# Kernel tuning notes

Measured on AMD Instinct MI355X. Metric: run time of the kernel, lower is better.

## Reference

```python
import jax, jax.numpy as jnp
import numpy as np

B, C, D, H, W = 4, 256, 16, 64, 64


def setup_inputs() -> dict:
    key = jax.random.key(0)
    ks = jax.random.split(key, 9)
    s = 1.0 / np.sqrt(C)
    return {
        "x": jax.random.normal(ks[0], (B, C, H, W), dtype=jnp.float32),
        "Wq": jax.random.normal(ks[1], (D, C), dtype=jnp.float32) * s,
        "bq": jax.random.normal(ks[2], (D,), dtype=jnp.float32) * 0.01,
        "Wk": jax.random.normal(ks[3], (D, C), dtype=jnp.float32) * s,
        "bk": jax.random.normal(ks[4], (D,), dtype=jnp.float32) * 0.01,
        "Wv": jax.random.normal(ks[5], (D, C), dtype=jnp.float32) * s,
        "bv": jax.random.normal(ks[6], (D,), dtype=jnp.float32) * 0.01,
        "Wo": jax.random.normal(ks[7], (C, D), dtype=jnp.float32) / np.sqrt(D),
        "bo": jax.random.normal(ks[8], (C,), dtype=jnp.float32) * 0.01,
    }


def reference(x, Wq, bq, Wk, bk, Wv, bv, Wo, bo):
    b, c, h, w = x.shape
    n = h * w
    xf = x.reshape(b, c, n)                                   # [B,C,N]
    # 1x1 convs == channel-mixing matmuls
    q = jnp.einsum("bcn,dc->bdn", xf, Wq) + bq[:, None]        # [B,D,N]
    k = jnp.einsum("bcn,dc->bdn", xf, Wk) + bk[:, None]
    v = jnp.einsum("bcn,dc->bdn", xf, Wv) + bv[:, None]
    # attention_map[b, i, j] = softmax_j(q_i . k_j)  (NO 1/sqrt(d) scale)
    scores = jnp.einsum("bdi,bdj->bij", q, k)                  # [B,N,N]
    attn = jax.nn.softmax(scores, axis=-1)
    # attended[b, d, i] = sum_j v[b,d,j] * attn[b,i,j]
    av = jnp.einsum("bdj,bij->bdi", v, attn)                   # [B,D,N]
    out = jnp.einsum("bdn,cd->bcn", av, Wo) + bo[:, None]      # [B,C,N]
    return out.reshape(b, c, h, w)
```

## Files before the change

### kernel.cpp

```cpp
#include <hip/hip_runtime.h>
#include <hip/hip_bf16.h>

typedef unsigned short u16;
typedef unsigned int u32;
typedef float f32x4 __attribute__((ext_vector_type(4)));
typedef short bf16x8 __attribute__((ext_vector_type(8)));

#define LOG2E 1.4426950408889634f

static __device__ __forceinline__ u16 f2bf(float f){
  __hip_bfloat16 h = __float2bfloat16(f);
  return __builtin_bit_cast(u16, h);
}
static __device__ __forceinline__ float bf2f(u16 u){
  __hip_bfloat16 h = __builtin_bit_cast(__hip_bfloat16, u);
  return __bfloat162float(h);
}
static __device__ __forceinline__ float fexp2(float x){
#if __has_builtin(__builtin_amdgcn_exp2f)
  return __builtin_amdgcn_exp2f(x);
#else
  return exp2f(x);
#endif
}
static __device__ __forceinline__ u32 pack2(float a, float b){
  return (u32)f2bf(a) | ((u32)f2bf(b) << 16);
}
static __device__ __forceinline__ f32x4 mf(bf16x8 a, bf16x8 b, f32x4 c){
  return __builtin_amdgcn_mfma_f32_16x16x32_bf16(a, b, c, 0, 0, 0);
}

__global__ __launch_bounds__(256, 2) void qkv_kernel(
    const float* __restrict__ x,
    const float* __restrict__ Wq, const float* __restrict__ bq,
    const float* __restrict__ Wk, const float* __restrict__ bk,
    const float* __restrict__ Wv, const float* __restrict__ bv,
    u16* __restrict__ qh, u16* __restrict__ ql,
    u16* __restrict__ kcat, u16* __restrict__ khz, u16* __restrict__ vT)
{
  __shared__ float wlds[48*256];
  int t = threadIdx.x;
  int nt = blockIdx.x, b = blockIdx.y;
  for (int idx = t; idx < 48*256; idx += 256) {
    int o = idx >> 8, c = idx & 255;
    int m = o >> 4, d = o & 15;
    const float* W = (m==0) ? Wq : (m==1) ? Wk : Wv;
    int cg = c >> 6, cc4 = (c >> 2) & 15, j = c & 3;
    int pos = (o << 8) + (cg << 6) + (((cc4 ^ cg) & 15) << 2) + j;
    wlds[pos] = W[d*256 + c];
  }
  __syncthreads();
  int w = t >> 6, lane = t & 63;
  int nl = lane & 15, cg = lane >> 4;
  int n = nt*64 + w*16 + nl;
  float acc[48];
  #pragma unroll
  for (int o = 0; o < 48; ++o) acc[o] = 0.f;
  const float* xb = x + (b << 20) + n;
  const float4* wl4 = (const float4*)wlds;
  #pragma unroll 2
  for (int cc4 = 0; cc4 < 16; ++cc4) {
    int c0 = cg*64 + cc4*4;
    float x0 = xb[(c0+0) << 12];
    float x1 = xb[(c0+1) << 12];
    float x2 = xb[(c0+2) << 12];
    float x3 = xb[(c0+3) << 12];
    int f4b = (cg << 4) + (cc4 ^ cg);
    #pragma unroll
    for (int o = 0; o < 48; ++o) {
      float4 wv = wl4[(o << 6) + f4b];
      acc[o] += wv.x*x0 + wv.y*x1 + wv.z*x2 + wv.w*x3;
    }
  }
  #pragma unroll
  for (int o = 0; o < 48; ++o) {
    acc[o] += __shfl_xor(acc[o], 16, 64);
    acc[o] += __shfl_xor(acc[o], 32, 64);
  }
  if (cg == 0) {
    alignas(16) u16 hq[16]; alignas(16) u16 lq[16];
    #pragma unroll
    for (int d = 0; d < 16; ++d) {
      float v_ = acc[d] + bq[d];
      u16 h = f2bf(v_);
      hq[d] = h;
      lq[d] = f2bf(v_ - bf2f(h));
    }
    int4* dst = (int4*)(qh + ((size_t)((b << 12) + n))*16);
    dst[0] = ((int4*)hq)[0]; dst[1] = ((int4*)hq)[1];
    int4* dst2 = (int4*)(ql + ((size_t)((b << 12) + n))*16);
    dst2[0] = ((int4*)lq)[0]; dst2[1] = ((int4*)lq)[1];
  } else if (cg == 1) {
    alignas(16) u16 kk[32]; alignas(16) u16 kz2[32];
    #pragma unroll
    for (int d = 0; d < 16; ++d) {
      float v_ = acc[16+d] + bk[d];
      u16 h = f2bf(v_);
      u16 l_ = f2bf(v_ - bf2f(h));
      kk[d] = h; kk[16+d] = l_;
      kz2[d] = h; kz2[16+d] = 0;
    }
    int4* dst = (int4*)(kcat + ((size_t)((b << 12) + n))*32);
    #pragma unroll
    for (int q_ = 0; q_ < 4; ++q_) dst[q_] = ((int4*)kk)[q_];
    int4* dst2 = (int4*)(khz + ((size_t)((b << 12) + n))*32);
    #pragma unroll
    for (int q_ = 0; q_ < 4; ++q_) dst2[q_] = ((int4*)kz2)[q_];
  } else if (cg == 2) {
    #pragma unroll
    for (int d = 0; d < 16; ++d) {
      float v_ = acc[32+d] + bv[d];
      vT[((size_t)((b*16 + d) << 12)) + n] = f2bf(v_);
    }
  }
}

struct Frags { bf16x8 ac0,ac1,ac2,ac3, az0,az1,az2,az3, v0,v1; };

static __device__ __forceinline__ Frags loadFrags(
  const u16* __restrict__ kc, const u16* __restrict__ kz,
  const u16* __restrict__ vp, int kb, int i, int g)
{
  Frags f;
  const u16* a0 = kc + (kb + i)*32 + g*8;
  f.ac0 = *(const bf16x8*)(a0);
  f.ac1 = *(const bf16x8*)(a0 + 512);
  f.ac2 = *(const bf16x8*)(a0 + 1024);
  f.ac3 = *(const bf16x8*)(a0 + 1536);
  const u16* z0 = kz + (kb + i)*32 + g*8;
  f.az0 = *(const bf16x8*)(z0);
  f.az1 = *(const bf16x8*)(z0 + 512);
  f.az2 = *(const bf16x8*)(z0 + 1024);
  f.az3 = *(const bf16x8*)(z0 + 1536);
  const u16* v0p = vp + kb + g*8;
  f.v0 = *(const bf16x8*)(v0p);
  f.v1 = *(const bf16x8*)(v0p + 32);
  return f;
}

__global__ __launch_bounds__(256, 2) void attn_kernel(
    const u16* __restrict__ qh, const u16* __restrict__ ql,
    const u16* __restrict__ kcat, const u16* __restrict__ khz,
    const u16* __restrict__ vT,
    float* __restrict__ av_part, float* __restrict__ l_part)
{
  __shared__ char plds[4*2048];
  int tid = threadIdx.x, wid = tid >> 6, lane = tid & 63;
  int g = lane >> 4, i = lane & 15;
  int b = blockIdx.y, s = blockIdx.z;
  int qidx = blockIdx.x*64 + wid*16 + i;
  char* myp = plds + wid*2048;
  int rowb = i*128;
  int mi = (i & 7) << 4;

  bf16x8 Bqh = *(const bf16x8*)(qh + ((size_t)((b << 12) + qidx))*16 + ((g & 1) << 3));
  bf16x8 Bql = *(const bf16x8*)(ql + ((size_t)((b << 12) + qidx))*16 + ((g & 1) << 3));
  const u16* kc = kcat + (size_t)b*4096*32;
  const u16* kz = khz  + (size_t)b*4096*32;
  const u16* vp = vT   + ((size_t)(b*16 + i) << 12);

  f32x4 av = {0.f,0.f,0.f,0.f};
  float lsum = 0.f;
  int kb0 = s*2048;
  Frags cu = loadFrags(kc, kz, vp, kb0, i, g);
  #pragma unroll 2
  for (int it = 0; it < 32; ++it) {
    int kb = kb0 + it*64;
    int kbn = (it < 31) ? (kb + 64) : kb;
    Frags nx = loadFrags(kc, kz, vp, kbn, i, g);
    f32x4 z4 = {0.f,0.f,0.f,0.f};
    f32x4 s0 = mf(cu.ac0, Bqh, z4); s0 = mf(cu.az0, Bql, s0);
    f32x4 s1 = mf(cu.ac1, Bqh, z4); s1 = mf(cu.az1, Bql, s1);
    f32x4 s2 = mf(cu.ac2, Bqh, z4); s2 = mf(cu.az2, Bql, s2);
    f32x4 s3 = mf(cu.ac3, Bqh, z4); s3 = mf(cu.az3, Bql, s3);
    f32x4 p0, p1, p2, p3;
    #pragma unroll
    for (int r = 0; r < 4; ++r) {
      p0[r] = fexp2(s0[r]*LOG2E);
      p1[r] = fexp2(s1[r]*LOG2E);
      p2[r] = fexp2(s2[r]*LOG2E);
      p3[r] = fexp2(s3[r]*LOG2E);
    }
    lsum += (p0[0]+p0[1]+p0[2]+p0[3]) + (p1[0]+p1[1]+p1[2]+p1[3])
          + (p2[0]+p2[1]+p2[2]+p2[3]) + (p3[0]+p3[1]+p3[2]+p3[3]);
    *(uint2*)(myp + rowb + (((8*g)      ) ^ mi)) =
        (uint2){ pack2(p0[0], p0[1]), pack2(p0[2], p0[3]) };
    *(uint2*)(myp + rowb + (((8*g) + 32 ) ^ mi)) =
        (uint2){ pack2(p1[0], p1[1]), pack2(p1[2], p1[3]) };
    *(uint2*)(myp + rowb + (((8*g) + 64 ) ^ mi)) =
        (uint2){ pack2(p2[0], p2[1]), pack2(p2[2], p2[3]) };
    *(uint2*)(myp + rowb + (((8*g) + 96 ) ^ mi)) =
        (uint2){ pack2(p3[0], p3[1]), pack2(p3[2], p3[3]) };
    bf16x8 Bp0 = *(const bf16x8*)(myp + rowb + (( 0 + 16*g) ^ mi));
    bf16x8 Bp1 = *(const bf16x8*)(myp + rowb + ((64 + 16*g) ^ mi));
    av = mf(cu.v0, Bp0, av);
    av = mf(cu.v1, Bp1, av);
    cu = nx;
  }
  float lt = lsum;
  lt += __shfl_xor(lt, 16, 64);
  lt += __shfl_xor(lt, 32, 64);
  float* avp = av_part + ((size_t)((s*4 + b)*16) << 12);
  #pragma unroll
  for (int r = 0; r < 4; ++r)
    avp[((size_t)(4*g + r) << 12) + qidx] = av[r];
  if (lane < 16)
    l_part[((size_t)((s*4 + b)) << 12) + qidx] = lt;
}

__global__ __launch_bounds__(256, 4) void outproj_kernel(
    const float* __restrict__ av_part, const float* __restrict__ l_part,
    const float* __restrict__ Wo, const float* __restrict__ bo,
    float* __restrict__ out)
{
  __shared__ float wl[16][16];
  __shared__ float bol[16];
  int t = threadIdx.x;
  int ct = blockIdx.x, ntile = blockIdx.y, b = blockIdx.z;
  wl[t >> 4][t & 15] = Wo[(ct*16 + (t >> 4))*16 + (t & 15)];
  if (t < 16) bol[t] = bo[ct*16 + t];
  __syncthreads();
  int n = ntile*256 + t;
  float l0 = l_part[((size_t)b << 12) + n];
  float l1 = l_part[((size_t)(4 + b) << 12) + n];
  float inv = 1.f / (l0 + l1);
  float avv[16];
  #pragma unroll
  for (int d = 0; d < 16; ++d) {
    float a0 = av_part[((size_t)(b*16 + d) << 12) + n];
    float a1 = av_part[((size_t)((4 + b)*16 + d) << 12) + n];
    avv[d] = (a0 + a1) * inv;
  }
  #pragma unroll
  for (int cc = 0; cc < 16; ++cc) {
    float o = bol[cc];
    #pragma unroll
    for (int d = 0; d < 16; ++d) o += wl[cc][d] * avv[d];
    out[((size_t)(b*256 + ct*16 + cc) << 12) + n] = o;
  }
}

extern "C" void kernel_launch(void* const* d_in, const int* in_sizes, int n_in,
                              void* d_out, int out_size, void* d_ws, size_t ws_size,
                              hipStream_t stream) {
  (void)in_sizes; (void)n_in; (void)out_size; (void)ws_size;
  const float* x  = (const float*)d_in[0];
  const float* Wq = (const float*)d_in[1];
  const float* bq = (const float*)d_in[2];
  const float* Wk = (const float*)d_in[3];
  const float* bk = (const float*)d_in[4];
  const float* Wv = (const float*)d_in[5];
  const float* bv = (const float*)d_in[6];
  const float* Wo = (const float*)d_in[7];
  const float* bo = (const float*)d_in[8];
  float* out = (float*)d_out;
  char* ws = (char*)d_ws;

  u16* qh   = (u16*)(ws + 0);
  u16* ql   = (u16*)(ws + 524288);
  u16* kcat = (u16*)(ws + 1048576);
  u16* khz  = (u16*)(ws + 2097152);
  u16* vT   = (u16*)(ws + 3145728);
  float* av_part = (float*)(ws + 3670016);
  float* l_part  = (float*)(ws + 5767168);

  qkv_kernel<<<dim3(64, 4), dim3(256), 0, stream>>>(
      x, Wq, bq, Wk, bk, Wv, bv, qh, ql, kcat, khz, vT);
  attn_kernel<<<dim3(64, 4, 2), dim3(256), 0, stream>>>(
      qh, ql, kcat, khz, vT, av_part, l_part);
  outproj_kernel<<<dim3(16, 16, 4), dim3(256), 0, stream>>>(
      av_part, l_part, Wo, bo, out);
}
```

Baseline: 159.5 us.

## Split QKV projection across grid, drop khz buffer, raise attention key-split count

The QKV kernel now launches one grid slice per projection (q, k, v), each holding only 16 output weights in LDS and 16 accumulators. This cuts register and LDS pressure and triples the block count. The separate zero-padded K buffer is removed: the attention kernel reuses the kcat fragments and zeroes the low-Q operand for the upper lane groups, which halves K fragment loads. The key dimension is split up to 8 ways, chosen from workspace size, and outproj reduces over a variable number of partial results, adding more partial-sum traffic in exchange for more parallel blocks.

```diff
diff --git a/kernel.cpp b/kernel.cpp
--- a/kernel.cpp
+++ b/kernel.cpp
@@ -36,29 +36,29 @@
     const float* __restrict__ Wk, const float* __restrict__ bk,
     const float* __restrict__ Wv, const float* __restrict__ bv,
     u16* __restrict__ qh, u16* __restrict__ ql,
-    u16* __restrict__ kcat, u16* __restrict__ khz, u16* __restrict__ vT)
-{
-  __shared__ float wlds[48*256];
+    u16* __restrict__ kcat, u16* __restrict__ vT)
+{
+  __shared__ float wlds[16*256];
   int t = threadIdx.x;
-  int nt = blockIdx.x, b = blockIdx.y;
-  for (int idx = t; idx < 48*256; idx += 256) {
-    int o = idx >> 8, c = idx & 255;
-    int m = o >> 4, d = o & 15;
-    const float* W = (m==0) ? Wq : (m==1) ? Wk : Wv;
+  int nt = blockIdx.x, b = blockIdx.y, m = blockIdx.z;
+  const float* W    = (m==0) ? Wq : (m==1) ? Wk : Wv;
+  const float* bias = (m==0) ? bq : (m==1) ? bk : bv;
+  for (int idx = t; idx < 16*256; idx += 256) {
+    int d = idx >> 8, c = idx & 255;
     int cg = c >> 6, cc4 = (c >> 2) & 15, j = c & 3;
-    int pos = (o << 8) + (cg << 6) + (((cc4 ^ cg) & 15) << 2) + j;
+    int pos = (d << 8) + (cg << 6) + ((cc4 ^ cg) << 2) + j;
     wlds[pos] = W[d*256 + c];
   }
   __syncthreads();
   int w = t >> 6, lane = t & 63;
   int nl = lane & 15, cg = lane >> 4;
   int n = nt*64 + w*16 + nl;
-  float acc[48];
-  #pragma unroll
-  for (int o = 0; o < 48; ++o) acc[o] = 0.f;
+  float acc[16];
+  #pragma unroll
+  for (int d = 0; d < 16; ++d) acc[d] = 0.f;
   const float* xb = x + (b << 20) + n;
   const float4* wl4 = (const float4*)wlds;
-  #pragma unroll 2
+  #pragma unroll 4
   for (int cc4 = 0; cc4 < 16; ++cc4) {
     int c0 = cg*64 + cc4*4;
     float x0 = xb[(c0+0) << 12];
@@ -67,59 +67,48 @@
     float x3 = xb[(c0+3) << 12];
     int f4b = (cg << 4) + (cc4 ^ cg);
     #pragma unroll
-    for (int o = 0; o < 48; ++o) {
-      float4 wv = wl4[(o << 6) + f4b];
-      acc[o] += wv.x*x0 + wv.y*x1 + wv.z*x2 + wv.w*x3;
-    }
-  }
-  #pragma unroll
-  for (int o = 0; o < 48; ++o) {
-    acc[o] += __shfl_xor(acc[o], 16, 64);
-    acc[o] += __shfl_xor(acc[o], 32, 64);
-  }
-  if (cg == 0) {
-    alignas(16) u16 hq[16]; alignas(16) u16 lq[16];
-    #pragma unroll
     for (int d = 0; d < 16; ++d) {
-      float v_ = acc[d] + bq[d];
+      float4 wv = wl4[(d << 6) + f4b];
+      acc[d] += wv.x*x0 + wv.y*x1 + wv.z*x2 + wv.w*x3;
+    }
+  }
+  #pragma unroll
+  for (int d = 0; d < 16; ++d) {
+    acc[d] += __shfl_xor(acc[d], 16, 64);
+    acc[d] += __shfl_xor(acc[d], 32, 64);
+  }
+  if (m == 2) {
+    #pragma unroll
+    for (int jj = 0; jj < 4; ++jj) {
+      int d = cg*4 + jj;
+      vT[((size_t)((b*16 + d)) << 12) + n] = f2bf(acc[d] + bias[d]);
+    }
+  } else {
+    int d0 = (cg & 1) * 8, lo = cg >> 1;
+    alignas(16) u16 vals[8];
+    #pragma unroll
+    for (int jj = 0; jj < 8; ++jj) {
+      int d = d0 + jj;
+      float v_ = acc[d] + bias[d];
       u16 h = f2bf(v_);
-      hq[d] = h;
-      lq[d] = f2bf(v_ - bf2f(h));
-    }
-    int4* dst = (int4*)(qh + ((size_t)((b << 12) + n))*16);
-    dst[0] = ((int4*)hq)[0]; dst[1] = ((int4*)hq)[1];
-    int4* dst2 = (int4*)(ql + ((size_t)((b << 12) + n))*16);
-    dst2[0] = ((int4*)lq)[0]; dst2[1] = ((int4*)lq)[1];
-  } else if (cg == 1) {
-    alignas(16) u16 kk[32]; alignas(16) u16 kz2[32];
-    #pragma unroll
-    for (int d = 0; d < 16; ++d) {
-      float v_ = acc[16+d] + bk[d];
-      u16 h = f2bf(v_);
-      u16 l_ = f2bf(v_ - bf2f(h));
-      kk[d] = h; kk[16+d] = l_;
-      kz2[d] = h; kz2[16+d] = 0;
-    }
-    int4* dst = (int4*)(kcat + ((size_t)((b << 12) + n))*32);
-    #pragma unroll
-    for (int q_ = 0; q_ < 4; ++q_) dst[q_] = ((int4*)kk)[q_];
-    int4* dst2 = (int4*)(khz + ((size_t)((b << 12) + n))*32);
-    #pragma unroll
-    for (int q_ = 0; q_ < 4; ++q_) dst2[q_] = ((int4*)kz2)[q_];
-  } else if (cg == 2) {
-    #pragma unroll
-    for (int d = 0; d < 16; ++d) {
-      float v_ = acc[32+d] + bv[d];
-      vT[((size_t)((b*16 + d) << 12)) + n] = f2bf(v_);
-    }
-  }
-}
-
-struct Frags { bf16x8 ac0,ac1,ac2,ac3, az0,az1,az2,az3, v0,v1; };
+      vals[jj] = lo ? f2bf(v_ - bf2f(h)) : h;
+    }
+    u16* dst;
+    if (m == 0) {
+      u16* base = lo ? ql : qh;
+      dst = base + (((size_t)(b << 12) + n) << 4) + d0;
+    } else {
+      dst = kcat + (((size_t)(b << 12) + n) << 5) + cg*8;
+    }
+    *(int4*)dst = *(const int4*)vals;
+  }
+}
+
+struct Frags { bf16x8 ac0,ac1,ac2,ac3, v0,v1; };
 
 static __device__ __forceinline__ Frags loadFrags(
-  const u16* __restrict__ kc, const u16* __restrict__ kz,
-  const u16* __restrict__ vp, int kb, int i, int g)
+  const u16* __restrict__ kc, const u16* __restrict__ vp,
+  int kb, int i, int g)
 {
   Frags f;
   const u16* a0 = kc + (kb + i)*32 + g*8;
@@ -127,11 +116,6 @@
   f.ac1 = *(const bf16x8*)(a0 + 512);
   f.ac2 = *(const bf16x8*)(a0 + 1024);
   f.ac3 = *(const bf16x8*)(a0 + 1536);
-  const u16* z0 = kz + (kb + i)*32 + g*8;
-  f.az0 = *(const bf16x8*)(z0);
-  f.az1 = *(const bf16x8*)(z0 + 512);
-  f.az2 = *(const bf16x8*)(z0 + 1024);
-  f.az3 = *(const bf16x8*)(z0 + 1536);
   const u16* v0p = vp + kb + g*8;
   f.v0 = *(const bf16x8*)(v0p);
   f.v1 = *(const bf16x8*)(v0p + 32);
@@ -140,14 +124,15 @@
 
 __global__ __launch_bounds__(256, 2) void attn_kernel(
     const u16* __restrict__ qh, const u16* __restrict__ ql,
-    const u16* __restrict__ kcat, const u16* __restrict__ khz,
-    const u16* __restrict__ vT,
+    const u16* __restrict__ kcat, const u16* __restrict__ vT,
     float* __restrict__ av_part, float* __restrict__ l_part)
 {
   __shared__ char plds[4*2048];
   int tid = threadIdx.x, wid = tid >> 6, lane = tid & 63;
   int g = lane >> 4, i = lane & 15;
   int b = blockIdx.y, s = blockIdx.z;
+  int nsplit = gridDim.z;
+  int iters = 64 / nsplit;
   int qidx = blockIdx.x*64 + wid*16 + i;
   char* myp = plds + wid*2048;
   int rowb = i*128;
@@ -155,24 +140,27 @@
 
   bf16x8 Bqh = *(const bf16x8*)(qh + ((size_t)((b << 12) + qidx))*16 + ((g & 1) << 3));
   bf16x8 Bql = *(const bf16x8*)(ql + ((size_t)((b << 12) + qidx))*16 + ((g & 1) << 3));
+  if (g >= 2) {
+    #pragma unroll
+    for (int e = 0; e < 8; ++e) Bql[e] = 0;
+  }
   const u16* kc = kcat + (size_t)b*4096*32;
-  const u16* kz = khz  + (size_t)b*4096*32;
   const u16* vp = vT   + ((size_t)(b*16 + i) << 12);
 
   f32x4 av = {0.f,0.f,0.f,0.f};
   float lsum = 0.f;
-  int kb0 = s*2048;
-  Frags cu = loadFrags(kc, kz, vp, kb0, i, g);
+  int kb0 = s*(iters*64);
+  Frags cu = loadFrags(kc, vp, kb0, i, g);
   #pragma unroll 2
-  for (int it = 0; it < 32; ++it) {
+  for (int it = 0; it < iters; ++it) {
     int kb = kb0 + it*64;
-    int kbn = (it < 31) ? (kb + 64) : kb;
-    Frags nx = loadFrags(kc, kz, vp, kbn, i, g);
+    int kbn = (it+1 < iters) ? (kb + 64) : kb;
+    Frags nx = loadFrags(kc, vp, kbn, i, g);
     f32x4 z4 = {0.f,0.f,0.f,0.f};
-    f32x4 s0 = mf(cu.ac0, Bqh, z4); s0 = mf(cu.az0, Bql, s0);
-    f32x4 s1 = mf(cu.ac1, Bqh, z4); s1 = mf(cu.az1, Bql, s1);
-    f32x4 s2 = mf(cu.ac2, Bqh, z4); s2 = mf(cu.az2, Bql, s2);
-    f32x4 s3 = mf(cu.ac3, Bqh, z4); s3 = mf(cu.az3, Bql, s3);
+    f32x4 s0 = mf(cu.ac0, Bqh, z4); s0 = mf(cu.ac0, Bql, s0);
+    f32x4 s1 = mf(cu.ac1, Bqh, z4); s1 = mf(cu.ac1, Bql, s1);
+    f32x4 s2 = mf(cu.ac2, Bqh, z4); s2 = mf(cu.ac2, Bql, s2);
+    f32x4 s3 = mf(cu.ac3, Bqh, z4); s3 = mf(cu.ac3, Bql, s3);
     f32x4 p0, p1, p2, p3;
     #pragma unroll
     for (int r = 0; r < 4; ++r) {
@@ -211,7 +199,7 @@
 __global__ __launch_bounds__(256, 4) void outproj_kernel(
     const float* __restrict__ av_part, const float* __restrict__ l_part,
     const float* __restrict__ Wo, const float* __restrict__ bo,
-    float* __restrict__ out)
+    float* __restrict__ out, int nsplit)
 {
   __shared__ float wl[16][16];
   __shared__ float bol[16];
@@ -221,16 +209,20 @@
   if (t < 16) bol[t] = bo[ct*16 + t];
   __syncthreads();
   int n = ntile*256 + t;
-  float l0 = l_part[((size_t)b << 12) + n];
-  float l1 = l_part[((size_t)(4 + b) << 12) + n];
-  float inv = 1.f / (l0 + l1);
+  float lsum = 0.f;
+  for (int s = 0; s < nsplit; ++s)
+    lsum += l_part[((size_t)(s*4 + b) << 12) + n];
+  float inv = 1.f / lsum;
   float avv[16];
   #pragma unroll
-  for (int d = 0; d < 16; ++d) {
-    float a0 = av_part[((size_t)(b*16 + d) << 12) + n];
-    float a1 = av_part[((size_t)((4 + b)*16 + d) << 12) + n];
-    avv[d] = (a0 + a1) * inv;
-  }
+  for (int d = 0; d < 16; ++d) avv[d] = 0.f;
+  for (int s = 0; s < nsplit; ++s) {
+    #pragma unroll
+    for (int d = 0; d < 16; ++d)
+      avv[d] += av_part[((size_t)((s*4 + b)*16 + d) << 12) + n];
+  }
+  #pragma unroll
+  for (int d = 0; d < 16; ++d) avv[d] *= inv;
   #pragma unroll
   for (int cc = 0; cc < 16; ++cc) {
     float o = bol[cc];
@@ -243,7 +235,7 @@
 extern "C" void kernel_launch(void* const* d_in, const int* in_sizes, int n_in,
                               void* d_out, int out_size, void* d_ws, size_t ws_size,
                               hipStream_t stream) {
-  (void)in_sizes; (void)n_in; (void)out_size; (void)ws_size;
+  (void)in_sizes; (void)n_in; (void)out_size;
   const float* x  = (const float*)d_in[0];
   const float* Wq = (const float*)d_in[1];
   const float* bq = (const float*)d_in[2];
@@ -256,18 +248,22 @@
   float* out = (float*)d_out;
   char* ws = (char*)d_ws;
 
+  const size_t fixed = 2621440;
+  const size_t per_split = 1048576 + 65536;
+  int nsplit = 8;
+  while (nsplit > 1 && fixed + (size_t)nsplit*per_split > ws_size) nsplit >>= 1;
+
   u16* qh   = (u16*)(ws + 0);
   u16* ql   = (u16*)(ws + 524288);
   u16* kcat = (u16*)(ws + 1048576);
-  u16* khz  = (u16*)(ws + 2097152);
-  u16* vT   = (u16*)(ws + 3145728);
-  float* av_part = (float*)(ws + 3670016);
-  float* l_part  = (float*)(ws + 5767168);
-
-  qkv_kernel<<<dim3(64, 4), dim3(256), 0, stream>>>(
-      x, Wq, bq, Wk, bk, Wv, bv, qh, ql, kcat, khz, vT);
-  attn_kernel<<<dim3(64, 4, 2), dim3(256), 0, stream>>>(
-      qh, ql, kcat, khz, vT, av_part, l_part);
+  u16* vT   = (u16*)(ws + 2097152);
+  float* av_part = (float*)(ws + fixed);
+  float* l_part  = (float*)(ws + fixed + (size_t)nsplit*1048576);
+
+  qkv_kernel<<<dim3(64, 4, 3), dim3(256), 0, stream>>>(
+      x, Wq, bq, Wk, bk, Wv, bv, qh, ql, kcat, vT);
+  attn_kernel<<<dim3(64, 4, nsplit), dim3(256), 0, stream>>>(
+      qh, ql, kcat, vT, av_part, l_part);
   outproj_kernel<<<dim3(16, 16, 4), dim3(256), 0, stream>>>(
-      av_part, l_part, Wo, bo, out);
-}
+      av_part, l_part, Wo, bo, out, nsplit);
+}
```

Result: faster. 151.8 us (-4.8%).
